# Kernel optimization log

Measured on AMD Instinct MI355X. Metric: run time of the kernel, lower is better.

Reference implementation:

```python
import jax, jax.numpy as jnp
import numpy as np

B, D, H = 16384, 1024, 1024
EPS = 1e-07


def setup_inputs() -> dict:
    key = jax.random.key(0)
    ks = jax.random.split(key, 16)
    s = 1.0 / np.sqrt(D)  # xavier-ish scale keeps exp() gate bounded
    mat = lambda k: (jax.random.normal(k, (D, H), dtype=jnp.float32) * s)
    zeros = lambda: jnp.zeros((H,), dtype=jnp.float32)
    return {
        "x": jax.random.normal(ks[0], (B, D), dtype=jnp.float32),
        "h_prev": jax.random.normal(ks[1], (B, H), dtype=jnp.float32) * 0.1,
        "c_prev": jax.random.normal(ks[2], (B, H), dtype=jnp.float32) * 0.1,
        "n_prev": jnp.ones((B, H), dtype=jnp.float32),
        "Wz": mat(ks[3]), "bWz": zeros(), "Rz": mat(ks[4]), "bRz": zeros(), "bz": zeros(),
        "Wi": mat(ks[5]), "bWi": zeros(), "Ri": mat(ks[6]), "bRi": zeros(), "bi": zeros(),
        "Wf": mat(ks[7]), "bWf": zeros(), "Rf": mat(ks[8]), "bRf": zeros(), "bf": zeros(),
        "Wo": mat(ks[9]), "bWo": zeros(), "Ro": mat(ks[10]), "bRo": zeros(), "bo": zeros(),
        "Wy": mat(ks[11]), "by": jnp.zeros((D,), dtype=jnp.float32),
    }


def reference(x, h_prev, c_prev, n_prev,
              Wz, bWz, Rz, bRz, bz,
              Wi, bWi, Ri, bRi, bi,
              Wf, bWf, Rf, bRf, bf,
              Wo, bWo, Ro, bRo, bo,
              Wy, by):
    # pre-activations: two fused GEMMs via concatenated weights
    Wcat = jnp.concatenate([Wz, Wi, Wf, Wo], axis=1)      # [D, 4H]
    Rcat = jnp.concatenate([Rz, Ri, Rf, Ro], axis=1)      # [H, 4H]
    bcat = jnp.concatenate([bWz + bRz + bz, bWi + bRi + bi,
                            bWf + bRf + bf, bWo + bRo + bo])
    pre = x @ Wcat + h_prev @ Rcat + bcat                  # [B, 4H]
    pz, pi, pf, po = jnp.split(pre, 4, axis=1)
    zt = jnp.tanh(pz)
    it = jnp.exp(pi)
    ft = jax.nn.sigmoid(pf)
    ot = jax.nn.sigmoid(po)
    C = ft * c_prev + it * zt
    n = ft * n_prev + it
    h = ot * jnp.tanh(C / (n + EPS))
    y = h @ Wy + by
    return y, (h, C, n)
```

## Files before the change

### kernel.cpp

```cpp
#include <hip/hip_runtime.h>
#include <math.h>
#include <stdint.h>


typedef __attribute__((ext_vector_type(8))) short bf16x8;
typedef __attribute__((ext_vector_type(4))) float f32x4;

constexpr int Bsz = 16384;
constexpr int Dd  = 1024;
constexpr int Hh  = 1024;
constexpr float EPSv = 1e-7f;

__device__ __forceinline__ unsigned short f2bf(float f) {
    union { float f; uint32_t u; } v; v.f = f;
    uint32_t u = v.u + 0x7fffu + ((v.u >> 16) & 1u);
    return (unsigned short)(u >> 16);
}

__device__ __forceinline__ void gload16(const void* g, void* l) {
    __builtin_amdgcn_global_load_lds(
        (const __attribute__((address_space(1))) void*)g,
        (__attribute__((address_space(3))) void*)l, 16, 0, 0);
}

__device__ __forceinline__ float sigm_f(float x) { return 1.f / (1.f + __expf(-x)); }
__device__ __forceinline__ float tanh_f(float x) {
    const float ax = fabsf(x);
    const float t = __expf(-2.f * ax);
    const float r = (1.f - t) / (1.f + t);
    return copysignf(r, x);
}


__global__ __launch_bounds__(256)
void cvt_A(const float* __restrict__ x, const float* __restrict__ hp, unsigned short* __restrict__ A)
{
    const int idx = blockIdx.x * 256 + threadIdx.x;
    const int n = idx * 8;
    const int b = n >> 11, k = n & 2047;
    const float* s = (k < 1024) ? (x + (size_t)b * 1024 + k)
                                : (hp + (size_t)b * 1024 + (k - 1024));
    const float4 v0 = *(const float4*)s;
    const float4 v1 = *(const float4*)(s + 4);
    union { unsigned short u[8]; uint4 v; } pk;
    pk.u[0] = f2bf(v0.x); pk.u[1] = f2bf(v0.y); pk.u[2] = f2bf(v0.z); pk.u[3] = f2bf(v0.w);
    pk.u[4] = f2bf(v1.x); pk.u[5] = f2bf(v1.y); pk.u[6] = f2bf(v1.z); pk.u[7] = f2bf(v1.w);
    *(uint4*)(A + n) = pk.v;
}

__global__ __launch_bounds__(256)
void cvt_T(const float* __restrict__ src, unsigned short* __restrict__ dst,
           int ldd, int kbase, int g, int mode)
{
    __shared__ float tile[64][65];
    const int t = threadIdx.x;
    const int kt = blockIdx.x & 15, jt = blockIdx.x >> 4;
    {
        const int lr = t >> 4, lc = (t & 15) * 4;
        #pragma unroll
        for (int rr = 0; rr < 64; rr += 16) {
            const float4 v = *(const float4*)(src + (size_t)(kt * 64 + rr + lr) * 1024 + jt * 64 + lc);
            tile[rr + lr][lc + 0] = v.x;
            tile[rr + lr][lc + 1] = v.y;
            tile[rr + lr][lc + 2] = v.z;
            tile[rr + lr][lc + 3] = v.w;
        }
    }
    __syncthreads();
    const int jl = t >> 2, kc = (t & 3) * 16;
    const int j = jt * 64 + jl;
    const int cp = mode ? j : ((j & 15) | (g << 4) | ((j >> 4) << 6));
    union { unsigned short u[16]; uint4 v[2]; } pk;
    #pragma unroll
    for (int q = 0; q < 16; ++q) pk.u[q] = f2bf(tile[kc + q][jl]);
    uint4* d = (uint4*)(dst + (size_t)cp * ldd + kbase + kt * 64 + kc);
    d[0] = pk.v[0];
    d[1] = pk.v[1];
}

__global__ __launch_bounds__(256)
void bias_sum(const float* bWz, const float* bRz, const float* bz,
              const float* bWi, const float* bRi, const float* bi,
              const float* bWf, const float* bRf, const float* bf_,
              const float* bWo, const float* bRo, const float* bo,
              float* __restrict__ bs)
{
    const int j = blockIdx.x * 256 + threadIdx.x;
    bs[j]        = bWz[j] + bRz[j] + bz[j];
    bs[1024 + j] = bWi[j] + bRi[j] + bi[j];
    bs[2048 + j] = bWf[j] + bRf[j] + bf_[j];
    bs[3072 + j] = bWo[j] + bRo[j] + bo[j];
}


template<int LD, int NTK, int NTILES, class Epi>
__device__ void mfma_core(const unsigned short* __restrict__ Ag,
                          const unsigned short* __restrict__ Bg,
                          int m0base, int n0, int t,
                          unsigned short* lds, Epi epi)
{
    constexpr int TOT = NTK * NTILES;
    const int lane = t & 63, wid = t >> 6;
    const int wr = wid >> 2, wc = wid & 3;
    const int cl = lane & 15, hi = lane >> 4;
    char* const L = (char*)lds;
    const int rdA0 = (wr * 128 + cl) * 128 + ((hi ^ (cl & 7)) << 4);
    const int rdB0 = 65536 + (wc * 64 + cl) * 128 + ((hi ^ (cl & 7)) << 4);
    const int srow = t >> 3;
    const int schk = ((t & 7) ^ (srow & 7)) * 8;
    const int sdst = t * 16;

    auto stgA = [&](int f, int buf) {
        const int ot = f / NTK, kt = f % NTK;
        const unsigned short* g = Ag + (size_t)(m0base + ot * 256 + srow) * LD + kt * 64 + schk;
        char* d = L + buf * 32768 + sdst;
        gload16(g,                  d);
        gload16(g + (size_t) 64 * LD, d + 8192);
        gload16(g + (size_t)128 * LD, d + 16384);
        gload16(g + (size_t)192 * LD, d + 24576);
    };
    auto stgB = [&](int f, int buf) {
        const int kt = f % NTK;
        const unsigned short* g = Bg + (size_t)(n0 + srow) * LD + kt * 64 + schk;
        char* d = L + 65536 + buf * 32768 + sdst;
        gload16(g,                  d);
        gload16(g + (size_t) 64 * LD, d + 8192);
        gload16(g + (size_t)128 * LD, d + 16384);
        gload16(g + (size_t)192 * LD, d + 24576);
    };

    f32x4 acc[8][4];
    #pragma unroll
    for (int i = 0; i < 8; ++i)
        #pragma unroll
        for (int j = 0; j < 4; ++j) acc[i][j] = (f32x4)0.f;

    stgA(0, 0); stgB(0, 0); stgB(1, 1);

    int bA = 0, bB = 0;
    for (int f = 0; f < TOT; ++f) {
        const int f1 = (f + 1 < TOT) ? f + 1 : TOT - 1;
        const int f2 = (f + 2 < TOT) ? f + 2 : TOT - 1;
        const int bB2 = (bB >= 1) ? bB - 1 : 2;

        __builtin_amdgcn_s_barrier();
        stgA(f1, bA ^ 1);
        stgB(f2, bB2);
        asm volatile("s_waitcnt vmcnt(12)" ::: "memory");

        const int aof = rdA0 + (bA << 15);
        const int bof = rdB0 + (bB << 15);
        bf16x8 a[8], b[4];

        #pragma unroll
        for (int mf = 0; mf < 8; ++mf) a[mf] = *(const bf16x8*)(L + aof + mf * 2048);
        #pragma unroll
        for (int nf = 0; nf < 4; ++nf) b[nf] = *(const bf16x8*)(L + bof + nf * 2048);
        #pragma unroll
        for (int mf = 0; mf < 8; ++mf)
            #pragma unroll
            for (int nf = 0; nf < 4; ++nf)
                acc[mf][nf] = __builtin_amdgcn_mfma_f32_16x16x32_bf16(a[mf], b[nf], acc[mf][nf], 0, 0, 0);

        #pragma unroll
        for (int mf = 0; mf < 8; ++mf) a[mf] = *(const bf16x8*)(L + (aof ^ 64) + mf * 2048);
        #pragma unroll
        for (int nf = 0; nf < 4; ++nf) b[nf] = *(const bf16x8*)(L + (bof ^ 64) + nf * 2048);
        #pragma unroll
        for (int mf = 0; mf < 8; ++mf)
            #pragma unroll
            for (int nf = 0; nf < 4; ++nf)
                acc[mf][nf] = __builtin_amdgcn_mfma_f32_16x16x32_bf16(a[mf], b[nf], acc[mf][nf], 0, 0, 0);

        if ((f % NTK) == NTK - 1) {
            epi(f / NTK, acc);
            #pragma unroll
            for (int i = 0; i < 8; ++i)
                #pragma unroll
                for (int j = 0; j < 4; ++j) acc[i][j] = (f32x4)0.f;
        }
        bA ^= 1;
        bB = (bB == 2) ? 0 : bB + 1;
    }
    asm volatile("s_waitcnt vmcnt(0)" ::: "memory");
}

__global__ __launch_bounds__(512, 2)
void gemm_gates(const unsigned short* __restrict__ A, const unsigned short* __restrict__ WT,
                const float* __restrict__ bsum,
                const float* __restrict__ c_prev, const float* __restrict__ n_prev,
                float* __restrict__ out_h, float* __restrict__ out_C, float* __restrict__ out_n,
                unsigned short* __restrict__ h_bf)
{
    __shared__ unsigned short lds[81920];
    const int t = threadIdx.x;
    const int b = blockIdx.x;
    const int nb  = (b & 7) * 2 + (b >> 7);
    const int mb0 = ((b >> 3) & 15) * 4;
    const int m0base = mb0 * 256;
    const int n0 = nb * 256;

    const int lane = t & 63, wid = t >> 6;
    const int wr = wid >> 2, wc = wid & 3;
    const int cl = lane & 15, hi = lane >> 4;
    const int j_out = nb * 64 + wc * 16 + cl;
    const float bz_ = bsum[j_out];
    const float bi_ = bsum[1024 + j_out];
    const float bf_ = bsum[2048 + j_out];
    const float bo_ = bsum[3072 + j_out];

    auto epi = [&](int ot, f32x4 (&acc)[8][4]) {
        #pragma unroll
        for (int mf = 0; mf < 8; ++mf) {
            const int rb = m0base + ot * 256 + wr * 128 + mf * 16 + hi * 4;
            #pragma unroll
            for (int r = 0; r < 4; ++r) {
                const size_t idx = (size_t)(rb + r) * 1024 + j_out;
                const float pz = acc[mf][0][r] + bz_;
                const float pi = acc[mf][1][r] + bi_;
                const float pf = acc[mf][2][r] + bf_;
                const float po = acc[mf][3][r] + bo_;
                const float zt = tanh_f(pz);
                const float it = __expf(pi);
                const float ft = sigm_f(pf);
                const float ot_ = sigm_f(po);
                const float Cv = ft * c_prev[idx] + it * zt;
                const float nv = ft * n_prev[idx] + it;
                const float hv = ot_ * tanh_f(Cv / (nv + EPSv));
                out_h[idx] = hv;
                out_C[idx] = Cv;
                out_n[idx] = nv;
                h_bf[idx] = f2bf(hv);
            }
        }
    };

    mfma_core<2048, 32, 4>(A, WT, m0base, n0, t, lds, epi);
}

__global__ __launch_bounds__(512, 2)
void gemm_y(const unsigned short* __restrict__ A, const unsigned short* __restrict__ WyT,
            const float* __restrict__ by, float* __restrict__ y)
{
    __shared__ unsigned short lds[81920];
    const int t = threadIdx.x;
    const int b = blockIdx.x;
    const int nb = b & 3, mb = b >> 2;
    const int m0base = mb * 256, n0 = nb * 256;

    const int lane = t & 63, wid = t >> 6;
    const int wr = wid >> 2, wc = wid & 3;
    const int cl = lane & 15, hi = lane >> 4;

    auto epi = [&](int ot, f32x4 (&acc)[8][4]) {
        (void)ot;
        #pragma unroll
        for (int mf = 0; mf < 8; ++mf) {
            const int rb = m0base + wr * 128 + mf * 16 + hi * 4;
            #pragma unroll
            for (int nf = 0; nf < 4; ++nf) {
                const int c = n0 + wc * 64 + nf * 16 + cl;
                const float bc = by[c];
                #pragma unroll
                for (int r = 0; r < 4; ++r)
                    y[(size_t)(rb + r) * 1024 + c] = acc[mf][nf][r] + bc;
            }
        }
    };

    mfma_core<1024, 16, 1>(A, WyT, m0base, n0, t, lds, epi);
}


constexpr int FBM = 64, FBN = 64, FBK = 16, FPAD = 4;

__global__ __launch_bounds__(256)
void fb_gates(const float* __restrict__ x, const float* __restrict__ h_prev,
              const float* __restrict__ c_prev, const float* __restrict__ n_prev,
              const float* __restrict__ Wz, const float* __restrict__ Rz,
              const float* __restrict__ Wi, const float* __restrict__ Ri,
              const float* __restrict__ Wf, const float* __restrict__ Rf,
              const float* __restrict__ Wo, const float* __restrict__ Ro,
              const float* __restrict__ bWz, const float* __restrict__ bRz, const float* __restrict__ bz,
              const float* __restrict__ bWi, const float* __restrict__ bRi, const float* __restrict__ bi,
              const float* __restrict__ bWf, const float* __restrict__ bRf, const float* __restrict__ bf_,
              const float* __restrict__ bWo, const float* __restrict__ bRo, const float* __restrict__ bo,
              float* __restrict__ out_h, float* __restrict__ out_C, float* __restrict__ out_n)
{
    __shared__ float sA[FBK][FBM + FPAD];
    __shared__ float sB[4][FBK][FBN + FPAD];
    const int t = threadIdx.x;
    const int col_blk = blockIdx.x & 15, row_blk = blockIdx.x >> 4;
    const int row0 = row_blk * FBM, col0 = col_blk * FBN;
    const int tx = t & 15, ty = t >> 4;
    float acc[4][4][4];
    #pragma unroll
    for (int g = 0; g < 4; ++g)
        for (int i = 0; i < 4; ++i)
            for (int j = 0; j < 4; ++j) acc[g][i][j] = 0.f;
    const int ar = t >> 2, ak = (t & 3) * 4, wk = t >> 4, wcc = (t & 15) * 4;
    for (int phase = 0; phase < 2; ++phase) {
        const float* Am = phase ? h_prev : x;
        const float* W0 = phase ? Rz : Wz; const float* W1 = phase ? Ri : Wi;
        const float* W2 = phase ? Rf : Wf; const float* W3 = phase ? Ro : Wo;
        for (int k0 = 0; k0 < 1024; k0 += FBK) {
            __syncthreads();
            {
                const float4 v = *(const float4*)(Am + (size_t)(row0 + ar) * 1024 + k0 + ak);
                sA[ak + 0][ar] = v.x; sA[ak + 1][ar] = v.y;
                sA[ak + 2][ar] = v.z; sA[ak + 3][ar] = v.w;
            }
            *(float4*)&sB[0][wk][wcc] = *(const float4*)(W0 + (size_t)(k0 + wk) * 1024 + col0 + wcc);
            *(float4*)&sB[1][wk][wcc] = *(const float4*)(W1 + (size_t)(k0 + wk) * 1024 + col0 + wcc);
            *(float4*)&sB[2][wk][wcc] = *(const float4*)(W2 + (size_t)(k0 + wk) * 1024 + col0 + wcc);
            *(float4*)&sB[3][wk][wcc] = *(const float4*)(W3 + (size_t)(k0 + wk) * 1024 + col0 + wcc);
            __syncthreads();
            #pragma unroll
            for (int kk = 0; kk < FBK; ++kk) {
                float a[4], bb[4][4];
                *(float4*)a = *(const float4*)&sA[kk][ty * 4];
                *(float4*)&bb[0][0] = *(const float4*)&sB[0][kk][tx * 4];
                *(float4*)&bb[1][0] = *(const float4*)&sB[1][kk][tx * 4];
                *(float4*)&bb[2][0] = *(const float4*)&sB[2][kk][tx * 4];
                *(float4*)&bb[3][0] = *(const float4*)&sB[3][kk][tx * 4];
                #pragma unroll
                for (int g = 0; g < 4; ++g)
                    for (int i = 0; i < 4; ++i)
                        for (int j = 0; j < 4; ++j)
                            acc[g][i][j] += a[i] * bb[g][j];
            }
        }
    }
    #pragma unroll
    for (int i = 0; i < 4; ++i) {
        const int r = row0 + ty * 4 + i;
        #pragma unroll
        for (int j = 0; j < 4; ++j) {
            const int c = col0 + tx * 4 + j;
            const float pz = acc[0][i][j] + bWz[c] + bRz[c] + bz[c];
            const float pi = acc[1][i][j] + bWi[c] + bRi[c] + bi[c];
            const float pf = acc[2][i][j] + bWf[c] + bRf[c] + bf_[c];
            const float po = acc[3][i][j] + bWo[c] + bRo[c] + bo[c];
            const float zt = tanhf(pz);
            const float it = expf(pi);
            const float ft = 1.f / (1.f + expf(-pf));
            const float ot = 1.f / (1.f + expf(-po));
            const size_t idx = (size_t)r * Hh + c;
            const float Cv = ft * c_prev[idx] + it * zt;
            const float nv = ft * n_prev[idx] + it;
            out_h[idx] = ot * tanhf(Cv / (nv + EPSv));
            out_C[idx] = Cv;
            out_n[idx] = nv;
        }
    }
}

__global__ __launch_bounds__(256)
void fb_ygemm(const float* __restrict__ hmat, const float* __restrict__ Wy,
              const float* __restrict__ by, float* __restrict__ y)
{
    __shared__ float sA[FBK][FBM + FPAD];
    __shared__ float sB[FBK][FBN + FPAD];
    const int t = threadIdx.x;
    const int col_blk = blockIdx.x & 15, row_blk = blockIdx.x >> 4;
    const int row0 = row_blk * FBM, col0 = col_blk * FBN;
    const int tx = t & 15, ty = t >> 4;
    float acc[4][4];
    #pragma unroll
    for (int i = 0; i < 4; ++i)
        for (int j = 0; j < 4; ++j) acc[i][j] = 0.f;
    const int ar = t >> 2, ak = (t & 3) * 4, wk = t >> 4, wcc = (t & 15) * 4;
    for (int k0 = 0; k0 < 1024; k0 += FBK) {
        __syncthreads();
        {
            const float4 v = *(const float4*)(hmat + (size_t)(row0 + ar) * 1024 + k0 + ak);
            sA[ak + 0][ar] = v.x; sA[ak + 1][ar] = v.y;
            sA[ak + 2][ar] = v.z; sA[ak + 3][ar] = v.w;
        }
        *(float4*)&sB[wk][wcc] = *(const float4*)(Wy + (size_t)(k0 + wk) * 1024 + col0 + wcc);
        __syncthreads();
        #pragma unroll
        for (int kk = 0; kk < FBK; ++kk) {
            float a[4], bb[4];
            *(float4*)a = *(const float4*)&sA[kk][ty * 4];
            *(float4*)bb = *(const float4*)&sB[kk][tx * 4];
            #pragma unroll
            for (int i = 0; i < 4; ++i)
                for (int j = 0; j < 4; ++j)
                    acc[i][j] += a[i] * bb[j];
        }
    }
    #pragma unroll
    for (int i = 0; i < 4; ++i) {
        const int r = row0 + ty * 4 + i;
        #pragma unroll
        for (int j = 0; j < 4; ++j) {
            const int c = col0 + tx * 4 + j;
            y[(size_t)r * Dd + c] = acc[i][j] + by[c];
        }
    }
}


extern "C" void kernel_launch(void* const* d_in, const int* in_sizes, int n_in,
                              void* d_out, int out_size, void* d_ws, size_t ws_size,
                              hipStream_t stream) {
    const float* x      = (const float*)d_in[0];
    const float* h_prev = (const float*)d_in[1];
    const float* c_prev = (const float*)d_in[2];
    const float* n_prev = (const float*)d_in[3];
    const float* Wz  = (const float*)d_in[4];
    const float* bWz = (const float*)d_in[5];
    const float* Rz  = (const float*)d_in[6];
    const float* bRz = (const float*)d_in[7];
    const float* bz  = (const float*)d_in[8];
    const float* Wi  = (const float*)d_in[9];
    const float* bWi = (const float*)d_in[10];
    const float* Ri  = (const float*)d_in[11];
    const float* bRi = (const float*)d_in[12];
    const float* bi  = (const float*)d_in[13];
    const float* Wf  = (const float*)d_in[14];
    const float* bWf = (const float*)d_in[15];
    const float* Rf  = (const float*)d_in[16];
    const float* bRf = (const float*)d_in[17];
    const float* bf_ = (const float*)d_in[18];
    const float* Wo  = (const float*)d_in[19];
    const float* bWo = (const float*)d_in[20];
    const float* Ro  = (const float*)d_in[21];
    const float* bRo = (const float*)d_in[22];
    const float* bo  = (const float*)d_in[23];
    const float* Wy  = (const float*)d_in[24];
    const float* by  = (const float*)d_in[25];

    float* y     = (float*)d_out;
    float* out_h = y + (size_t)Bsz * Dd;
    float* out_C = out_h + (size_t)Bsz * Hh;
    float* out_n = out_C + (size_t)Bsz * Hh;

    const size_t OFF_A    = 0;
    const size_t OFF_WT   = 67108864;
    const size_t OFF_WYT  = 83886080;
    const size_t OFF_HBF  = 85983232;
    const size_t OFF_BS   = 119537664;
    const size_t WS_NEED  = 119554048;

    if (ws_size >= WS_NEED) {
        char* ws = (char*)d_ws;
        unsigned short* A_bf = (unsigned short*)(ws + OFF_A);
        unsigned short* WT   = (unsigned short*)(ws + OFF_WT);
        unsigned short* WyT  = (unsigned short*)(ws + OFF_WYT);
        unsigned short* h_bf = (unsigned short*)(ws + OFF_HBF);
        float* bsum          = (float*)(ws + OFF_BS);

        cvt_A<<<16384, 256, 0, stream>>>(x, h_prev, A_bf);
        cvt_T<<<256, 256, 0, stream>>>(Wz, WT, 2048, 0,    0, 0);
        cvt_T<<<256, 256, 0, stream>>>(Rz, WT, 2048, 1024, 0, 0);
        cvt_T<<<256, 256, 0, stream>>>(Wi, WT, 2048, 0,    1, 0);
        cvt_T<<<256, 256, 0, stream>>>(Ri, WT, 2048, 1024, 1, 0);
        cvt_T<<<256, 256, 0, stream>>>(Wf, WT, 2048, 0,    2, 0);
        cvt_T<<<256, 256, 0, stream>>>(Rf, WT, 2048, 1024, 2, 0);
        cvt_T<<<256, 256, 0, stream>>>(Wo, WT, 2048, 0,    3, 0);
        cvt_T<<<256, 256, 0, stream>>>(Ro, WT, 2048, 1024, 3, 0);
        cvt_T<<<256, 256, 0, stream>>>(Wy, WyT, 1024, 0,   0, 1);
        bias_sum<<<4, 256, 0, stream>>>(bWz, bRz, bz, bWi, bRi, bi,
                                        bWf, bRf, bf_, bWo, bRo, bo, bsum);

        gemm_gates<<<256, 512, 0, stream>>>(A_bf, WT, bsum, c_prev, n_prev,
                                            out_h, out_C, out_n, h_bf);
        gemm_y<<<256, 512, 0, stream>>>(h_bf, WyT, by, y);
    } else {
        dim3 block(256);
        dim3 grid((Bsz / FBM) * (Hh / FBN));
        fb_gates<<<grid, block, 0, stream>>>(x, h_prev, c_prev, n_prev,
                                             Wz, Rz, Wi, Ri, Wf, Rf, Wo, Ro,
                                             bWz, bRz, bz, bWi, bRi, bi,
                                             bWf, bRf, bf_, bWo, bRo, bo,
                                             out_h, out_C, out_n);
        fb_ygemm<<<grid, block, 0, stream>>>(out_h, Wy, by, y);
    }
}
```

Before: 439.0 us.

## Merge weight conversion launches and hand-schedule LDS reads around MFMA loops

After: 425.6 us. 1.03x faster.

```diff
diff --git a/kernel.cpp b/kernel.cpp
--- a/kernel.cpp
+++ b/kernel.cpp
@@ -30,6 +30,8 @@
     const float r = (1.f - t) / (1.f + t);
     return copysignf(r, x);
 }
+
+#define DSR(d, a, o) asm volatile("ds_read_b128 %0, %1 offset:" o : "=v"(d) : "v"(a) : "memory")
 
 
 __global__ __launch_bounds__(256)
@@ -48,13 +50,31 @@
     *(uint4*)(A + n) = pk.v;
 }
 
+struct CvtArgs {
+    const float* src[9];
+    const float* bptr[12];
+    unsigned short* wt;
+    unsigned short* wyt;
+    float* bs;
+};
+
 __global__ __launch_bounds__(256)
-void cvt_T(const float* __restrict__ src, unsigned short* __restrict__ dst,
-           int ldd, int kbase, int g, int mode)
+void cvt_W(CvtArgs P)
 {
     __shared__ float tile[64][65];
+    const int bid = blockIdx.x;
     const int t = threadIdx.x;
-    const int kt = blockIdx.x & 15, jt = blockIdx.x >> 4;
+    if (bid >= 2304) {
+        const int j = (bid - 2304) * 256 + t;
+        P.bs[j]        = P.bptr[0][j] + P.bptr[1][j]  + P.bptr[2][j];
+        P.bs[1024 + j] = P.bptr[3][j] + P.bptr[4][j]  + P.bptr[5][j];
+        P.bs[2048 + j] = P.bptr[6][j] + P.bptr[7][j]  + P.bptr[8][j];
+        P.bs[3072 + j] = P.bptr[9][j] + P.bptr[10][j] + P.bptr[11][j];
+        return;
+    }
+    const int id = bid >> 8, sub = bid & 255;
+    const float* __restrict__ src = P.src[id];
+    const int kt = sub & 15, jt = sub >> 4;
     {
         const int lr = t >> 4, lc = (t & 15) * 4;
         #pragma unroll
@@ -69,27 +89,19 @@
     __syncthreads();
     const int jl = t >> 2, kc = (t & 3) * 16;
     const int j = jt * 64 + jl;
-    const int cp = mode ? j : ((j & 15) | (g << 4) | ((j >> 4) << 6));
     union { unsigned short u[16]; uint4 v[2]; } pk;
     #pragma unroll
     for (int q = 0; q < 16; ++q) pk.u[q] = f2bf(tile[kc + q][jl]);
-    uint4* d = (uint4*)(dst + (size_t)cp * ldd + kbase + kt * 64 + kc);
+    uint4* d;
+    if (id == 8) {
+        d = (uint4*)(P.wyt + (size_t)j * 1024 + kt * 64 + kc);
+    } else {
+        const int g = id >> 1, kbase = (id & 1) ? 1024 : 0;
+        const int cp = (j & 15) | (g << 4) | ((j >> 4) << 6);
+        d = (uint4*)(P.wt + (size_t)cp * 2048 + kbase + kt * 64 + kc);
+    }
     d[0] = pk.v[0];
     d[1] = pk.v[1];
-}
-
-__global__ __launch_bounds__(256)
-void bias_sum(const float* bWz, const float* bRz, const float* bz,
-              const float* bWi, const float* bRi, const float* bi,
-              const float* bWf, const float* bRf, const float* bf_,
-              const float* bWo, const float* bRo, const float* bo,
-              float* __restrict__ bs)
-{
-    const int j = blockIdx.x * 256 + threadIdx.x;
-    bs[j]        = bWz[j] + bRz[j] + bz[j];
-    bs[1024 + j] = bWi[j] + bRi[j] + bi[j];
-    bs[2048 + j] = bWf[j] + bRf[j] + bf_[j];
-    bs[3072 + j] = bWo[j] + bRo[j] + bo[j];
 }
 
 
@@ -103,12 +115,13 @@
     const int lane = t & 63, wid = t >> 6;
     const int wr = wid >> 2, wc = wid & 3;
     const int cl = lane & 15, hi = lane >> 4;
-    char* const L = (char*)lds;
-    const int rdA0 = (wr * 128 + cl) * 128 + ((hi ^ (cl & 7)) << 4);
-    const int rdB0 = 65536 + (wc * 64 + cl) * 128 + ((hi ^ (cl & 7)) << 4);
+    const int Lb = (int)(size_t)(__attribute__((address_space(3))) unsigned short*)lds;
+    const int rdA0 = Lb + (wr * 128 + cl) * 128 + ((hi ^ (cl & 7)) << 4);
+    const int rdB0 = Lb + 65536 + (wc * 64 + cl) * 128 + ((hi ^ (cl & 7)) << 4);
     const int srow = t >> 3;
     const int schk = ((t & 7) ^ (srow & 7)) * 8;
     const int sdst = t * 16;
+    char* const L = (char*)lds;
 
     auto stgA = [&](int f, int buf) {
         const int ot = f / NTK, kt = f % NTK;
@@ -143,34 +156,48 @@
         const int f2 = (f + 2 < TOT) ? f + 2 : TOT - 1;
         const int bB2 = (bB >= 1) ? bB - 1 : 2;
 
+        asm volatile("s_waitcnt vmcnt(4)" ::: "memory");
         __builtin_amdgcn_s_barrier();
         stgA(f1, bA ^ 1);
         stgB(f2, bB2);
-        asm volatile("s_waitcnt vmcnt(12)" ::: "memory");
-
-        const int aof = rdA0 + (bA << 15);
-        const int bof = rdB0 + (bB << 15);
-        bf16x8 a[8], b[4];
-
-        #pragma unroll
-        for (int mf = 0; mf < 8; ++mf) a[mf] = *(const bf16x8*)(L + aof + mf * 2048);
-        #pragma unroll
-        for (int nf = 0; nf < 4; ++nf) b[nf] = *(const bf16x8*)(L + bof + nf * 2048);
+
+        const int aof  = rdA0 + (bA << 15);
+        const int bof  = rdB0 + (bB << 15);
+        const int aof1 = aof ^ 64;
+        const int bof1 = bof ^ 64;
+        bf16x8 a0[8], b0[4], a1[8], b1[4];
+
+        DSR(a0[0], aof, "0");     DSR(a0[1], aof, "2048");
+        DSR(a0[2], aof, "4096");  DSR(a0[3], aof, "6144");
+        DSR(a0[4], aof, "8192");  DSR(a0[5], aof, "10240");
+        DSR(a0[6], aof, "12288"); DSR(a0[7], aof, "14336");
+        DSR(b0[0], bof, "0");     DSR(b0[1], bof, "2048");
+        DSR(b0[2], bof, "4096");  DSR(b0[3], bof, "6144");
+        DSR(a1[0], aof1, "0");     DSR(a1[1], aof1, "2048");
+        DSR(a1[2], aof1, "4096");  DSR(a1[3], aof1, "6144");
+        DSR(a1[4], aof1, "8192");  DSR(a1[5], aof1, "10240");
+        DSR(a1[6], aof1, "12288"); DSR(a1[7], aof1, "14336");
+
+        asm volatile("s_waitcnt lgkmcnt(8)" ::: "memory");
+        __builtin_amdgcn_sched_barrier(0);
+        __builtin_amdgcn_s_setprio(1);
         #pragma unroll
         for (int mf = 0; mf < 8; ++mf)
             #pragma unroll
             for (int nf = 0; nf < 4; ++nf)
-                acc[mf][nf] = __builtin_amdgcn_mfma_f32_16x16x32_bf16(a[mf], b[nf], acc[mf][nf], 0, 0, 0);
-
-        #pragma unroll
-        for (int mf = 0; mf < 8; ++mf) a[mf] = *(const bf16x8*)(L + (aof ^ 64) + mf * 2048);
-        #pragma unroll
-        for (int nf = 0; nf < 4; ++nf) b[nf] = *(const bf16x8*)(L + (bof ^ 64) + nf * 2048);
+                acc[mf][nf] = __builtin_amdgcn_mfma_f32_16x16x32_bf16(a0[mf], b0[nf], acc[mf][nf], 0, 0, 0);
+
+        DSR(b1[0], bof1, "0");    DSR(b1[1], bof1, "2048");
+        DSR(b1[2], bof1, "4096"); DSR(b1[3], bof1, "6144");
+
+        asm volatile("s_waitcnt lgkmcnt(0)" ::: "memory");
+        __builtin_amdgcn_sched_barrier(0);
         #pragma unroll
         for (int mf = 0; mf < 8; ++mf)
             #pragma unroll
             for (int nf = 0; nf < 4; ++nf)
-                acc[mf][nf] = __builtin_amdgcn_mfma_f32_16x16x32_bf16(a[mf], b[nf], acc[mf][nf], 0, 0, 0);
+                acc[mf][nf] = __builtin_amdgcn_mfma_f32_16x16x32_bf16(a1[mf], b1[nf], acc[mf][nf], 0, 0, 0);
+        __builtin_amdgcn_s_setprio(0);
 
         if ((f % NTK) == NTK - 1) {
             epi(f / NTK, acc);
@@ -453,17 +480,16 @@
         float* bsum          = (float*)(ws + OFF_BS);
 
         cvt_A<<<16384, 256, 0, stream>>>(x, h_prev, A_bf);
-        cvt_T<<<256, 256, 0, stream>>>(Wz, WT, 2048, 0,    0, 0);
-        cvt_T<<<256, 256, 0, stream>>>(Rz, WT, 2048, 1024, 0, 0);
-        cvt_T<<<256, 256, 0, stream>>>(Wi, WT, 2048, 0,    1, 0);
-        cvt_T<<<256, 256, 0, stream>>>(Ri, WT, 2048, 1024, 1, 0);
-        cvt_T<<<256, 256, 0, stream>>>(Wf, WT, 2048, 0,    2, 0);
-        cvt_T<<<256, 256, 0, stream>>>(Rf, WT, 2048, 1024, 2, 0);
-        cvt_T<<<256, 256, 0, stream>>>(Wo, WT, 2048, 0,    3, 0);
-        cvt_T<<<256, 256, 0, stream>>>(Ro, WT, 2048, 1024, 3, 0);
-        cvt_T<<<256, 256, 0, stream>>>(Wy, WyT, 1024, 0,   0, 1);
-        bias_sum<<<4, 256, 0, stream>>>(bWz, bRz, bz, bWi, bRi, bi,
-                                        bWf, bRf, bf_, bWo, bRo, bo, bsum);
+
+        CvtArgs P;
+        P.src[0] = Wz; P.src[1] = Rz; P.src[2] = Wi; P.src[3] = Ri;
+        P.src[4] = Wf; P.src[5] = Rf; P.src[6] = Wo; P.src[7] = Ro; P.src[8] = Wy;
+        P.bptr[0] = bWz; P.bptr[1] = bRz; P.bptr[2]  = bz;
+        P.bptr[3] = bWi; P.bptr[4] = bRi; P.bptr[5]  = bi;
+        P.bptr[6] = bWf; P.bptr[7] = bRf; P.bptr[8]  = bf_;
+        P.bptr[9] = bWo; P.bptr[10] = bRo; P.bptr[11] = bo;
+        P.wt = WT; P.wyt = WyT; P.bs = bsum;
+        cvt_W<<<2308, 256, 0, stream>>>(P);
 
         gemm_gates<<<256, 512, 0, stream>>>(A_bf, WT, bsum, c_prev, n_prev,
                                             out_h, out_C, out_n, h_bf);
```
